# Performance work log

Hardware: AMD Instinct MI355X
Metric: run time of the kernel (lower is better)

The kernel has to match this reference:

```python
import jax, jax.numpy as jnp
import numpy as np

D_IN = 2048
D_OUT = 2048
BOUND = 1.0


def setup_inputs() -> dict:
    key = jax.random.key(0)
    kx, kw = jax.random.split(key)
    x = jax.random.normal(kx, (4, 2048, D_IN), dtype=jnp.float32)
    W_raw = 0.02 * jax.random.normal(kw, (D_OUT, D_IN), dtype=jnp.float32)
    return {"x": x, "W_raw": W_raw}


def reference(x, W_raw):
    # sigma = ||W||_2 (largest singular value), exact via SVD
    sigma = jnp.linalg.svd(W_raw, full_matrices=False, compute_uv=False)[0]
    scale = jnp.maximum(sigma / BOUND, 1.0)  # clamp(sigma/bound, min=1)
    Wn = W_raw / scale                        # [d_out, d_in]
    return jnp.einsum('bsi,oi->bso', x, Wn)   # x @ Wn.T
```

## Files before the change

kernel.cpp:

```cpp
#include <hip/hip_runtime.h>
#include <stdint.h>

typedef short bf16x8 __attribute__((ext_vector_type(8)));
typedef float f32x4 __attribute__((ext_vector_type(4)));

__device__ __forceinline__ unsigned short f2bf(float f) {
  union { float f; unsigned int u; } v; v.f = f;
  unsigned int u = v.u;
  return (unsigned short)((u + 0x7FFFu + ((u >> 16) & 1u)) >> 16);
}
__device__ __forceinline__ float bf2f(unsigned short u) {
  union { unsigned int u; float f; } v; v.u = ((unsigned int)u) << 16;
  return v.f;
}
__device__ __forceinline__ void async16(const void* g, void* l) {
  __builtin_amdgcn_global_load_lds(
      (const __attribute__((address_space(1))) unsigned int*)g,
      (__attribute__((address_space(3))) unsigned int*)l, 16, 0, 0);
}

__global__ __launch_bounds__(256) void cast_f32_bf16(
    const float* __restrict__ in, unsigned short* __restrict__ out, int n8) {
  int i = blockIdx.x * 256 + threadIdx.x;
  if (i >= n8) return;
  const float4* p = (const float4*)in;
  float4 a = p[2 * (size_t)i], b = p[2 * (size_t)i + 1];
  union { bf16x8 v; unsigned short s[8]; } o;
  o.s[0] = f2bf(a.x); o.s[1] = f2bf(a.y); o.s[2] = f2bf(a.z); o.s[3] = f2bf(a.w);
  o.s[4] = f2bf(b.x); o.s[5] = f2bf(b.y); o.s[6] = f2bf(b.z); o.s[7] = f2bf(b.w);
  *(bf16x8*)(out + 8 * (size_t)i) = o.v;
}

__device__ __forceinline__ void stage16k(const unsigned short* __restrict__ g0,
                                         int ldK, unsigned short* lds, int tid) {
#pragma unroll
  for (int q = 0; q < 2; ++q) {
    int idx = q * 512 + tid;
    int r = idx >> 3;
    int jj = (idx & 7) ^ (r & 7);
    async16(g0 + (size_t)r * ldK + jj * 8,
            lds + ((size_t)(q * 512 + (tid & ~63))) * 8);
  }
}

template <int OMODE>
__global__ __launch_bounds__(512, 2) void gemm256(
    const unsigned short* __restrict__ A, const unsigned short* __restrict__ B,
    void* __restrict__ Cv, int M, int N, int lda, int K,
    int nTn, int mT, const float* __restrict__ scale_ptr) {
  __shared__ __align__(16) unsigned short AsBuf[3][256 * 64];
  __shared__ __align__(16) unsigned short BsBuf[2][256 * 64];
  const int tid = threadIdx.x;
  const int w = tid >> 6, lane = tid & 63;
  int bid = blockIdx.x;
  const int mb = bid % mT; bid /= mT;
  const int nb = bid % nTn; const int ks = bid / nTn;
  const int m0 = mb * 256, n0 = nb * 256;
  const int wr = w >> 2, wc = w & 3;
  const int R = K >> 7;

  const unsigned short* Ab = A + (size_t)m0 * lda + (size_t)ks * K;
  const unsigned short* Bb = B + (size_t)n0 * lda + (size_t)ks * K;

  unsigned short *a0 = AsBuf[0], *a1 = AsBuf[1], *a2 = AsBuf[2];
  unsigned short *b0 = BsBuf[0], *b1 = BsBuf[1];

  stage16k(Ab,                          lda, a0,            tid);
  stage16k(Ab + (size_t)128 * lda,      lda, a0 + 128 * 64, tid);
  stage16k(Bb,                          lda, b0,            tid);
  stage16k(Bb + (size_t)128 * lda,      lda, b0 + 128 * 64, tid);
  stage16k(Ab + 64,                     lda, a1,            tid);
  stage16k(Ab + 64 + (size_t)128 * lda, lda, a1 + 128 * 64, tid);
  stage16k(Bb + 64,                     lda, b1,            tid);
  stage16k(Bb + 64 + (size_t)128 * lda, lda, b1 + 128 * 64, tid);
  asm volatile("s_waitcnt vmcnt(8)" ::: "memory");
  __builtin_amdgcn_s_barrier();
  asm volatile("" ::: "memory");

  const int fr = lane & 15;
  const int bc0 = ((lane >> 4) << 4) ^ ((fr & 7) << 4);
  const int bc1 = bc0 ^ 64;

  f32x4 acc[8][4] = {};

  for (int r = 0; r < R; ++r) {
    const bool st = (r + 1 < R);
    bf16x8 bg[4][2];
#pragma unroll
    for (int ph = 0; ph < 8; ++ph) {
      const int d = ph >> 2, q = ph & 3;
      const char* cA = (const char*)(d == 0 ? a0 : a1);
      const char* cB = (const char*)(d == 0 ? b0 : b1);
      if (q == 0) {
#pragma unroll
        for (int nf = 0; nf < 4; ++nf) {
          int rb = (wc * 64 + nf * 16 + fr) * 128;
          bg[nf][0] = *(const bf16x8*)(cB + rb + bc0);
          bg[nf][1] = *(const bf16x8*)(cB + rb + bc1);
        }
      }
      bf16x8 af[2][2];
#pragma unroll
      for (int m2 = 0; m2 < 2; ++m2) {
        int rb = (wr * 128 + q * 32 + m2 * 16 + fr) * 128;
        af[m2][0] = *(const bf16x8*)(cA + rb + bc0);
        af[m2][1] = *(const bf16x8*)(cA + rb + bc1);
      }
      if (st) switch (ph) {
        case 0: stage16k(Ab + (size_t)(2 * r + 2) * 64, lda, a2, tid); break;
        case 1: stage16k(Ab + (size_t)(2 * r + 2) * 64 + (size_t)128 * lda, lda,
                         a2 + 128 * 64, tid); break;
        case 2: stage16k(Bb + (size_t)(2 * r + 2) * 64, lda, b0, tid); break;
        case 3: stage16k(Bb + (size_t)(2 * r + 2) * 64 + (size_t)128 * lda, lda,
                         b0 + 128 * 64, tid); break;
        case 4: stage16k(Ab + (size_t)(2 * r + 3) * 64, lda, a0, tid); break;
        case 5: stage16k(Ab + (size_t)(2 * r + 3) * 64 + (size_t)128 * lda, lda,
                         a0 + 128 * 64, tid); break;
        case 6: stage16k(Bb + (size_t)(2 * r + 3) * 64, lda, b1, tid); break;
        case 7: stage16k(Bb + (size_t)(2 * r + 3) * 64 + (size_t)128 * lda, lda,
                         b1 + 128 * 64, tid); break;
      }
      asm volatile("" ::: "memory");
      __builtin_amdgcn_s_barrier();
      asm volatile("" ::: "memory");
      __builtin_amdgcn_s_setprio(1);
#pragma unroll
      for (int m2 = 0; m2 < 2; ++m2)
#pragma unroll
        for (int nf = 0; nf < 4; ++nf)
#pragma unroll
          for (int kh = 0; kh < 2; ++kh)
            acc[q * 2 + m2][nf] = __builtin_amdgcn_mfma_f32_16x16x32_bf16(
                af[m2][kh], bg[nf][kh], acc[q * 2 + m2][nf], 0, 0, 0);
      __builtin_amdgcn_s_setprio(0);
      asm volatile("" ::: "memory");
      if (ph == 3) {
        if (st) asm volatile("s_waitcnt vmcnt(8)" ::: "memory");
        else    asm volatile("s_waitcnt vmcnt(0)" ::: "memory");
      } else if (ph == 7) {
        if (st) asm volatile("s_waitcnt vmcnt(8)" ::: "memory");
      }
      __builtin_amdgcn_s_barrier();
      asm volatile("" ::: "memory");
    }
    unsigned short* t = a2; a2 = a1; a1 = a0; a0 = t;
  }

  float sc = 1.0f;
  if (OMODE == 1) sc = *scale_ptr;
  size_t base = (OMODE == 2) ? (size_t)ks * ((size_t)M * N) : 0;
  const int rr0 = m0 + wr * 128 + ((lane >> 4) << 2);
  const int cc0 = n0 + wc * 64 + fr;
#pragma unroll
  for (int mf = 0; mf < 8; ++mf)
#pragma unroll
    for (int nf = 0; nf < 4; ++nf)
#pragma unroll
      for (int tt = 0; tt < 4; ++tt) {
        size_t idx = base + (size_t)(rr0 + mf * 16 + tt) * N + (cc0 + nf * 16);
        if (OMODE == 2) ((unsigned short*)Cv)[idx] = f2bf(acc[mf][nf][tt]);
        else            ((float*)Cv)[idx] = acc[mf][nf][tt] * sc;
      }
}

__global__ __launch_bounds__(256) void reduce_planes_init(
    const unsigned short* __restrict__ P, unsigned short* __restrict__ out,
    int n8, int np, size_t plane, float* __restrict__ t0,
    float* __restrict__ czero) {
  int i = blockIdx.x * 256 + threadIdx.x;
  if (blockIdx.x < 8) {
    int j = blockIdx.x * 256 + threadIdx.x;
    unsigned int h = (unsigned int)j * 2654435761u;
    h ^= h >> 16; h *= 2246822519u; h ^= h >> 13;
    t0[j] = (float)(h & 0xFFFFu) * (1.0f / 65536.0f) - 0.5f;
    if (j == 0) czero[0] = 0.0f;
  }
  if (i >= n8) return;
  float s[8] = {0.f, 0.f, 0.f, 0.f, 0.f, 0.f, 0.f, 0.f};
  for (int p = 0; p < np; ++p) {
    bf16x8 v = *(const bf16x8*)(P + (size_t)p * plane + (size_t)i * 8);
#pragma unroll
    for (int j = 0; j < 8; ++j) s[j] += bf2f((unsigned short)v[j]);
  }
  union { bf16x8 v; unsigned short u[8]; } o;
#pragma unroll
  for (int j = 0; j < 8; ++j) o.u[j] = f2bf(s[j]);
  *(bf16x8*)(out + (size_t)i * 8) = o.v;
}

__global__ __launch_bounds__(256) void power_step_bf16(
    const unsigned short* __restrict__ Am, const float* __restrict__ tin,
    float* __restrict__ tout, const float* __restrict__ cptr) {
  __shared__ __align__(16) float vs[2048];
  __shared__ float wred[4];
  const int tid = threadIdx.x;
  float4 x0 = ((const float4*)tin)[2 * tid];
  float4 x1 = ((const float4*)tin)[2 * tid + 1];
  float ss = x0.x * x0.x + x0.y * x0.y + x0.z * x0.z + x0.w * x0.w +
             x1.x * x1.x + x1.y * x1.y + x1.z * x1.z + x1.w * x1.w;
#pragma unroll
  for (int o = 32; o > 0; o >>= 1) ss += __shfl_xor(ss, o);
  if ((tid & 63) == 0) wred[tid >> 6] = ss;
  __syncthreads();
  float inv = 1.0f / sqrtf(wred[0] + wred[1] + wred[2] + wred[3]);
  float4* vp = (float4*)vs;
  float4 y0 = {x0.x * inv, x0.y * inv, x0.z * inv, x0.w * inv};
  float4 y1 = {x1.x * inv, x1.y * inv, x1.z * inv, x1.w * inv};
  vp[2 * tid] = y0;
  vp[2 * tid + 1] = y1;
  __syncthreads();
  const int row = blockIdx.x * 8 + (tid >> 5);
  const int sub = tid & 31;
  const bf16x8* Ar = (const bf16x8*)(Am + (size_t)row * 2048);
  float s = 0.f;
#pragma unroll 2
  for (int c = sub; c < 256; c += 32) {
    bf16x8 a = Ar[c];
    float4 v0 = vp[2 * c], v1 = vp[2 * c + 1];
    s += bf2f((unsigned short)a[0]) * v0.x + bf2f((unsigned short)a[1]) * v0.y +
         bf2f((unsigned short)a[2]) * v0.z + bf2f((unsigned short)a[3]) * v0.w +
         bf2f((unsigned short)a[4]) * v1.x + bf2f((unsigned short)a[5]) * v1.y +
         bf2f((unsigned short)a[6]) * v1.z + bf2f((unsigned short)a[7]) * v1.w;
  }
#pragma unroll
  for (int o = 16; o > 0; o >>= 1) s += __shfl_xor(s, o);
  if (sub == 0) tout[row] = s - cptr[0] * vs[row];
}

__global__ __launch_bounds__(256) void finalize_rough(
    const float* __restrict__ tk, float* __restrict__ cout) {
  __shared__ float wred[4];
  const int tid = threadIdx.x;
  float4 x0 = ((const float4*)tk)[2 * tid];
  float4 x1 = ((const float4*)tk)[2 * tid + 1];
  float ss = x0.x * x0.x + x0.y * x0.y + x0.z * x0.z + x0.w * x0.w +
             x1.x * x1.x + x1.y * x1.y + x1.z * x1.z + x1.w * x1.w;
#pragma unroll
  for (int o = 32; o > 0; o >>= 1) ss += __shfl_xor(ss, o);
  if ((tid & 63) == 0) wred[tid >> 6] = ss;
  __syncthreads();
  if (tid == 0)
    cout[0] = 0.49f * sqrtf(wred[0] + wred[1] + wred[2] + wred[3]);
}

__global__ __launch_bounds__(256) void finalize_sigma(
    const float* __restrict__ tk, const float* __restrict__ cptr,
    float* __restrict__ inv_scale) {
  __shared__ float wred[4];
  const int tid = threadIdx.x;
  float4 x0 = ((const float4*)tk)[2 * tid];
  float4 x1 = ((const float4*)tk)[2 * tid + 1];
  float ss = x0.x * x0.x + x0.y * x0.y + x0.z * x0.z + x0.w * x0.w +
             x1.x * x1.x + x1.y * x1.y + x1.z * x1.z + x1.w * x1.w;
#pragma unroll
  for (int o = 32; o > 0; o >>= 1) ss += __shfl_xor(ss, o);
  if ((tid & 63) == 0) wred[tid >> 6] = ss;
  __syncthreads();
  if (tid == 0) {
    float lam = sqrtf(wred[0] + wred[1] + wred[2] + wred[3]) + cptr[0];
    float sigma = sqrtf(lam);
    float scl = fmaxf(sigma, 1.0f);
    inv_scale[0] = 1.0f / scl;
  }
}

extern "C" void kernel_launch(void* const* d_in, const int* in_sizes, int n_in,
                              void* d_out, int out_size, void* d_ws, size_t ws_size,
                              hipStream_t stream) {
  (void)in_sizes; (void)n_in; (void)out_size; (void)ws_size;
  const float* x = (const float*)d_in[0];
  const float* W = (const float*)d_in[1];
  float* out = (float*)d_out;
  char* ws = (char*)d_ws;
  const int K = 2048, N = 2048, M = 4 * 2048;
  const size_t PLANE = (size_t)2048 * 2048;

  unsigned short* xb = (unsigned short*)(ws);
  unsigned short* Wb = (unsigned short*)(ws + ((size_t)32 << 20));
  unsigned short* P1 = (unsigned short*)(ws + ((size_t)40 << 20));
  unsigned short* Am = P1;
  float* tv = (float*)(ws + ((size_t)72 << 20));
  float* inv_scale = tv + 4096;
  float* czero = tv + 4097;
  float* cshift = tv + 4098;

  cast_f32_bf16<<<(M * K / 8 + 255) / 256, 256, 0, stream>>>(x, xb, M * K / 8);
  cast_f32_bf16<<<(N * K / 8 + 255) / 256, 256, 0, stream>>>(W, Wb, N * K / 8);

  gemm256<2><<<256, 512, 0, stream>>>(Wb, Wb, P1, 2048, 2048, 2048, 512, 8, 8, nullptr);
  reduce_planes_init<<<2048, 256, 0, stream>>>(P1, Am, (int)(PLANE / 8), 4, PLANE,
                                               tv, czero);

  int s = 0;
  for (; s < 5; ++s)
    power_step_bf16<<<256, 256, 0, stream>>>(Am, tv + (s & 1) * 2048,
                                             tv + ((s + 1) & 1) * 2048, czero);
  finalize_rough<<<1, 256, 0, stream>>>(tv + (s & 1) * 2048, cshift);
  for (; s < 22; ++s)
    power_step_bf16<<<256, 256, 0, stream>>>(Am, tv + (s & 1) * 2048,
                                             tv + ((s + 1) & 1) * 2048, cshift);
  finalize_sigma<<<1, 256, 0, stream>>>(tv + (s & 1) * 2048, cshift, inv_scale);

  gemm256<1><<<256, 512, 0, stream>>>(xb, Wb, out, M, N, K, K, 8, 32, inv_scale);
}
```

Baseline: 198.2 us.

## Use 32x32 MFMA tiles in GEMM and fuse power iterations into persistent kernel

The GEMM inner loop now uses 32x32x16 bf16 MFMA instructions with 16-wide accumulators in place of 16x16x32, and the fragment addressing and epilogue are rewritten to match. This lowers the instruction count and register pressure per tile. Separately, the 22 power-iteration launches plus two finalize kernels are replaced by one persistent kernel that uses a global atomic counter as a grid barrier between iterations, removing per-launch overhead. The grid barrier depends on all 256 blocks being co-resident, and if they are not it can deadlock.

```diff
diff --git a/kernel.cpp b/kernel.cpp
--- a/kernel.cpp
+++ b/kernel.cpp
@@ -3,6 +3,7 @@
 
 typedef short bf16x8 __attribute__((ext_vector_type(8)));
 typedef float f32x4 __attribute__((ext_vector_type(4)));
+typedef float f32x16 __attribute__((ext_vector_type(16)));
 
 __device__ __forceinline__ unsigned short f2bf(float f) {
   union { float f; unsigned int u; } v; v.f = f;
@@ -77,15 +78,14 @@
   __builtin_amdgcn_s_barrier();
   asm volatile("" ::: "memory");
 
-  const int fr = lane & 15;
-  const int bc0 = ((lane >> 4) << 4) ^ ((fr & 7) << 4);
-  const int bc1 = bc0 ^ 64;
-
-  f32x4 acc[8][4] = {};
+  const int l31 = lane & 31, lhi = lane >> 5;
+  const int sa = l31 & 7;
+
+  f32x16 acc[4][2] = {};
 
   for (int r = 0; r < R; ++r) {
     const bool st = (r + 1 < R);
-    bf16x8 bg[4][2];
+    bf16x8 bg[2][4];
 #pragma unroll
     for (int ph = 0; ph < 8; ++ph) {
       const int d = ph >> 2, q = ph & 3;
@@ -93,19 +93,18 @@
       const char* cB = (const char*)(d == 0 ? b0 : b1);
       if (q == 0) {
 #pragma unroll
-        for (int nf = 0; nf < 4; ++nf) {
-          int rb = (wc * 64 + nf * 16 + fr) * 128;
-          bg[nf][0] = *(const bf16x8*)(cB + rb + bc0);
-          bg[nf][1] = *(const bf16x8*)(cB + rb + bc1);
+        for (int nt = 0; nt < 2; ++nt) {
+          const char* pb = cB + (wc * 64 + nt * 32 + l31) * 128;
+#pragma unroll
+          for (int ks2 = 0; ks2 < 4; ++ks2)
+            bg[nt][ks2] = *(const bf16x8*)(pb + (((ks2 * 2 + lhi) ^ sa) << 4));
         }
       }
-      bf16x8 af[2][2];
-#pragma unroll
-      for (int m2 = 0; m2 < 2; ++m2) {
-        int rb = (wr * 128 + q * 32 + m2 * 16 + fr) * 128;
-        af[m2][0] = *(const bf16x8*)(cA + rb + bc0);
-        af[m2][1] = *(const bf16x8*)(cA + rb + bc1);
-      }
+      bf16x8 af[4];
+      const char* pa = cA + (wr * 128 + q * 32 + l31) * 128;
+#pragma unroll
+      for (int ks2 = 0; ks2 < 4; ++ks2)
+        af[ks2] = *(const bf16x8*)(pa + (((ks2 * 2 + lhi) ^ sa) << 4));
       if (st) switch (ph) {
         case 0: stage16k(Ab + (size_t)(2 * r + 2) * 64, lda, a2, tid); break;
         case 1: stage16k(Ab + (size_t)(2 * r + 2) * 64 + (size_t)128 * lda, lda,
@@ -125,13 +124,11 @@
       asm volatile("" ::: "memory");
       __builtin_amdgcn_s_setprio(1);
 #pragma unroll
-      for (int m2 = 0; m2 < 2; ++m2)
-#pragma unroll
-        for (int nf = 0; nf < 4; ++nf)
-#pragma unroll
-          for (int kh = 0; kh < 2; ++kh)
-            acc[q * 2 + m2][nf] = __builtin_amdgcn_mfma_f32_16x16x32_bf16(
-                af[m2][kh], bg[nf][kh], acc[q * 2 + m2][nf], 0, 0, 0);
+      for (int ks2 = 0; ks2 < 4; ++ks2)
+#pragma unroll
+        for (int nt = 0; nt < 2; ++nt)
+          acc[q][nt] = __builtin_amdgcn_mfma_f32_32x32x16_bf16(
+              af[ks2], bg[nt][ks2], acc[q][nt], 0, 0, 0);
       __builtin_amdgcn_s_setprio(0);
       asm volatile("" ::: "memory");
       if (ph == 3) {
@@ -149,31 +146,32 @@
   float sc = 1.0f;
   if (OMODE == 1) sc = *scale_ptr;
   size_t base = (OMODE == 2) ? (size_t)ks * ((size_t)M * N) : 0;
-  const int rr0 = m0 + wr * 128 + ((lane >> 4) << 2);
-  const int cc0 = n0 + wc * 64 + fr;
-#pragma unroll
-  for (int mf = 0; mf < 8; ++mf)
-#pragma unroll
-    for (int nf = 0; nf < 4; ++nf)
-#pragma unroll
-      for (int tt = 0; tt < 4; ++tt) {
-        size_t idx = base + (size_t)(rr0 + mf * 16 + tt) * N + (cc0 + nf * 16);
-        if (OMODE == 2) ((unsigned short*)Cv)[idx] = f2bf(acc[mf][nf][tt]);
-        else            ((float*)Cv)[idx] = acc[mf][nf][tt] * sc;
+  const int rr0 = m0 + wr * 128 + lhi * 4;
+  const int cc0 = n0 + wc * 64 + l31;
+#pragma unroll
+  for (int q = 0; q < 4; ++q)
+#pragma unroll
+    for (int nt = 0; nt < 2; ++nt)
+#pragma unroll
+      for (int reg = 0; reg < 16; ++reg) {
+        int row = rr0 + q * 32 + (reg & 3) + 8 * (reg >> 2);
+        size_t idx = base + (size_t)row * N + (cc0 + nt * 32);
+        if (OMODE == 2) ((unsigned short*)Cv)[idx] = f2bf(acc[q][nt][reg]);
+        else            ((float*)Cv)[idx] = acc[q][nt][reg] * sc;
       }
 }
 
 __global__ __launch_bounds__(256) void reduce_planes_init(
     const unsigned short* __restrict__ P, unsigned short* __restrict__ out,
     int n8, int np, size_t plane, float* __restrict__ t0,
-    float* __restrict__ czero) {
+    unsigned* __restrict__ cnt) {
   int i = blockIdx.x * 256 + threadIdx.x;
   if (blockIdx.x < 8) {
     int j = blockIdx.x * 256 + threadIdx.x;
     unsigned int h = (unsigned int)j * 2654435761u;
     h ^= h >> 16; h *= 2246822519u; h ^= h >> 13;
     t0[j] = (float)(h & 0xFFFFu) * (1.0f / 65536.0f) - 0.5f;
-    if (j == 0) czero[0] = 0.0f;
+    if (j == 0) cnt[0] = 0u;
   }
   if (i >= n8) return;
   float s[8] = {0.f, 0.f, 0.f, 0.f, 0.f, 0.f, 0.f, 0.f};
@@ -188,79 +186,81 @@
   *(bf16x8*)(out + (size_t)i * 8) = o.v;
 }
 
-__global__ __launch_bounds__(256) void power_step_bf16(
-    const unsigned short* __restrict__ Am, const float* __restrict__ tin,
-    float* __restrict__ tout, const float* __restrict__ cptr) {
+__global__ __launch_bounds__(256) void power_persist(
+    const unsigned short* __restrict__ Am, float* __restrict__ tv,
+    unsigned* __restrict__ cnt, float* __restrict__ inv_scale) {
   __shared__ __align__(16) float vs[2048];
   __shared__ float wred[4];
   const int tid = threadIdx.x;
-  float4 x0 = ((const float4*)tin)[2 * tid];
-  float4 x1 = ((const float4*)tin)[2 * tid + 1];
-  float ss = x0.x * x0.x + x0.y * x0.y + x0.z * x0.z + x0.w * x0.w +
-             x1.x * x1.x + x1.y * x1.y + x1.z * x1.z + x1.w * x1.w;
-#pragma unroll
-  for (int o = 32; o > 0; o >>= 1) ss += __shfl_xor(ss, o);
-  if ((tid & 63) == 0) wred[tid >> 6] = ss;
-  __syncthreads();
-  float inv = 1.0f / sqrtf(wred[0] + wred[1] + wred[2] + wred[3]);
-  float4* vp = (float4*)vs;
-  float4 y0 = {x0.x * inv, x0.y * inv, x0.z * inv, x0.w * inv};
-  float4 y1 = {x1.x * inv, x1.y * inv, x1.z * inv, x1.w * inv};
-  vp[2 * tid] = y0;
-  vp[2 * tid + 1] = y1;
-  __syncthreads();
   const int row = blockIdx.x * 8 + (tid >> 5);
   const int sub = tid & 31;
   const bf16x8* Ar = (const bf16x8*)(Am + (size_t)row * 2048);
-  float s = 0.f;
+  float c = 0.0f;
+
+  for (int it = 0; it < 22; ++it) {
+    const float* tin = tv + (it & 1) * 2048;
+    float* tout = tv + ((it + 1) & 1) * 2048;
+    float xv[8];
+#pragma unroll
+    for (int j = 0; j < 8; ++j)
+      xv[j] = __hip_atomic_load(&tin[tid * 8 + j], __ATOMIC_RELAXED,
+                                __HIP_MEMORY_SCOPE_AGENT);
+    float ss = 0.f;
+#pragma unroll
+    for (int j = 0; j < 8; ++j) ss += xv[j] * xv[j];
+#pragma unroll
+    for (int o = 32; o > 0; o >>= 1) ss += __shfl_xor(ss, o);
+    if ((tid & 63) == 0) wred[tid >> 6] = ss;
+    __syncthreads();
+    float nrm = sqrtf(wred[0] + wred[1] + wred[2] + wred[3]);
+    if (it == 5) c = 0.49f * nrm;
+    float inv = 1.0f / nrm;
+#pragma unroll
+    for (int j = 0; j < 8; ++j) vs[tid * 8 + j] = xv[j] * inv;
+    __syncthreads();
+    float s = 0.f;
 #pragma unroll 2
-  for (int c = sub; c < 256; c += 32) {
-    bf16x8 a = Ar[c];
-    float4 v0 = vp[2 * c], v1 = vp[2 * c + 1];
-    s += bf2f((unsigned short)a[0]) * v0.x + bf2f((unsigned short)a[1]) * v0.y +
-         bf2f((unsigned short)a[2]) * v0.z + bf2f((unsigned short)a[3]) * v0.w +
-         bf2f((unsigned short)a[4]) * v1.x + bf2f((unsigned short)a[5]) * v1.y +
-         bf2f((unsigned short)a[6]) * v1.z + bf2f((unsigned short)a[7]) * v1.w;
-  }
-#pragma unroll
-  for (int o = 16; o > 0; o >>= 1) s += __shfl_xor(s, o);
-  if (sub == 0) tout[row] = s - cptr[0] * vs[row];
-}
-
-__global__ __launch_bounds__(256) void finalize_rough(
-    const float* __restrict__ tk, float* __restrict__ cout) {
-  __shared__ float wred[4];
-  const int tid = threadIdx.x;
-  float4 x0 = ((const float4*)tk)[2 * tid];
-  float4 x1 = ((const float4*)tk)[2 * tid + 1];
-  float ss = x0.x * x0.x + x0.y * x0.y + x0.z * x0.z + x0.w * x0.w +
-             x1.x * x1.x + x1.y * x1.y + x1.z * x1.z + x1.w * x1.w;
-#pragma unroll
-  for (int o = 32; o > 0; o >>= 1) ss += __shfl_xor(ss, o);
-  if ((tid & 63) == 0) wred[tid >> 6] = ss;
-  __syncthreads();
-  if (tid == 0)
-    cout[0] = 0.49f * sqrtf(wred[0] + wred[1] + wred[2] + wred[3]);
-}
-
-__global__ __launch_bounds__(256) void finalize_sigma(
-    const float* __restrict__ tk, const float* __restrict__ cptr,
-    float* __restrict__ inv_scale) {
-  __shared__ float wred[4];
-  const int tid = threadIdx.x;
-  float4 x0 = ((const float4*)tk)[2 * tid];
-  float4 x1 = ((const float4*)tk)[2 * tid + 1];
-  float ss = x0.x * x0.x + x0.y * x0.y + x0.z * x0.z + x0.w * x0.w +
-             x1.x * x1.x + x1.y * x1.y + x1.z * x1.z + x1.w * x1.w;
-#pragma unroll
-  for (int o = 32; o > 0; o >>= 1) ss += __shfl_xor(ss, o);
-  if ((tid & 63) == 0) wred[tid >> 6] = ss;
-  __syncthreads();
-  if (tid == 0) {
-    float lam = sqrtf(wred[0] + wred[1] + wred[2] + wred[3]) + cptr[0];
-    float sigma = sqrtf(lam);
-    float scl = fmaxf(sigma, 1.0f);
-    inv_scale[0] = 1.0f / scl;
+    for (int cc = sub; cc < 256; cc += 32) {
+      bf16x8 a = Ar[cc];
+      float4 v0 = ((const float4*)vs)[2 * cc], v1 = ((const float4*)vs)[2 * cc + 1];
+      s += bf2f((unsigned short)a[0]) * v0.x + bf2f((unsigned short)a[1]) * v0.y +
+           bf2f((unsigned short)a[2]) * v0.z + bf2f((unsigned short)a[3]) * v0.w +
+           bf2f((unsigned short)a[4]) * v1.x + bf2f((unsigned short)a[5]) * v1.y +
+           bf2f((unsigned short)a[6]) * v1.z + bf2f((unsigned short)a[7]) * v1.w;
+    }
+#pragma unroll
+    for (int o = 16; o > 0; o >>= 1) s += __shfl_xor(s, o);
+    if (sub == 0)
+      __hip_atomic_store(&tout[row], s - c * vs[row], __ATOMIC_RELAXED,
+                         __HIP_MEMORY_SCOPE_AGENT);
+    __syncthreads();
+    if (tid == 0) {
+      __threadfence();
+      __hip_atomic_fetch_add(cnt, 1u, __ATOMIC_ACQ_REL, __HIP_MEMORY_SCOPE_AGENT);
+      const unsigned tgt = (unsigned)(it + 1) * gridDim.x;
+      while (__hip_atomic_load(cnt, __ATOMIC_ACQUIRE, __HIP_MEMORY_SCOPE_AGENT) < tgt)
+        __builtin_amdgcn_s_sleep(2);
+    }
+    __syncthreads();
+  }
+
+  if (blockIdx.x == 0) {
+    float ss = 0.f;
+#pragma unroll
+    for (int j = 0; j < 8; ++j) {
+      float v = __hip_atomic_load(&tv[tid * 8 + j], __ATOMIC_RELAXED,
+                                  __HIP_MEMORY_SCOPE_AGENT);
+      ss += v * v;
+    }
+#pragma unroll
+    for (int o = 32; o > 0; o >>= 1) ss += __shfl_xor(ss, o);
+    if ((tid & 63) == 0) wred[tid >> 6] = ss;
+    __syncthreads();
+    if (tid == 0) {
+      float lam = sqrtf(wred[0] + wred[1] + wred[2] + wred[3]) + c;
+      float sigma = sqrtf(lam);
+      inv_scale[0] = 1.0f / fmaxf(sigma, 1.0f);
+    }
   }
 }
 
@@ -281,25 +281,16 @@
   unsigned short* Am = P1;
   float* tv = (float*)(ws + ((size_t)72 << 20));
   float* inv_scale = tv + 4096;
-  float* czero = tv + 4097;
-  float* cshift = tv + 4098;
+  unsigned* cnt = (unsigned*)(tv + 4104);
 
   cast_f32_bf16<<<(M * K / 8 + 255) / 256, 256, 0, stream>>>(x, xb, M * K / 8);
   cast_f32_bf16<<<(N * K / 8 + 255) / 256, 256, 0, stream>>>(W, Wb, N * K / 8);
 
   gemm256<2><<<256, 512, 0, stream>>>(Wb, Wb, P1, 2048, 2048, 2048, 512, 8, 8, nullptr);
   reduce_planes_init<<<2048, 256, 0, stream>>>(P1, Am, (int)(PLANE / 8), 4, PLANE,
-                                               tv, czero);
-
-  int s = 0;
-  for (; s < 5; ++s)
-    power_step_bf16<<<256, 256, 0, stream>>>(Am, tv + (s & 1) * 2048,
-                                             tv + ((s + 1) & 1) * 2048, czero);
-  finalize_rough<<<1, 256, 0, stream>>>(tv + (s & 1) * 2048, cshift);
-  for (; s < 22; ++s)
-    power_step_bf16<<<256, 256, 0, stream>>>(Am, tv + (s & 1) * 2048,
-                                             tv + ((s + 1) & 1) * 2048, cshift);
-  finalize_sigma<<<1, 256, 0, stream>>>(tv + (s & 1) * 2048, cshift, inv_scale);
+                                               tv, cnt);
+
+  power_persist<<<256, 256, 0, stream>>>(Am, tv, cnt, inv_scale);
 
   gemm256<1><<<256, 512, 0, stream>>>(xb, Wb, out, M, N, K, K, 8, 32, inv_scale);
 }
```

Result: slower. 609.0 us (+207.3%).
